# Performance work log

Hardware: AMD Instinct MI355X
Metric: run time of the kernel (lower is better)

## Reference

```python
import jax, jax.numpy as jnp
import numpy as np
from jax import lax

DN = ('NCHW', 'OIHW', 'NCHW')

def _hard_sigmoid(x):
    return jnp.clip(0.2 * x + 0.5, 0.0, 1.0)

def _conv(x, k, pad):
    return lax.conv_general_dilated(x, k, (1, 1), pad, dimension_numbers=DN)

def setup_inputs() -> dict:
    key = jax.random.key(0)
    k1, k2, k3 = jax.random.split(key, 3)
    B, T, C, H, W = 8, 16, 8, 128, 128
    F = 32
    x = jax.random.normal(k1, (B, T, C, H, W), dtype=jnp.float32)
    Wk = jax.random.normal(k2, (4 * F, C, 3, 3), dtype=jnp.float32) * 0.05
    Uk = jax.random.normal(k3, (4 * F, F, 3, 3), dtype=jnp.float32) * 0.05
    b = jnp.zeros((4 * F,), dtype=jnp.float32)
    return {"x": x, "Wk": Wk, "Uk": Uk, "b": b}

def reference(x, Wk, Uk, b):
    # ConvLSTM2D, channels_first, valid padding on input conv, same on recurrent conv,
    # gate order i,f,c,o; activation=tanh, recurrent_activation=hard_sigmoid.
    B, T, C, H, W = x.shape
    F = Uk.shape[1]
    kh, kw = Wk.shape[2], Wk.shape[3]
    Ho, Wo = H - kh + 1, W - kw + 1  # valid padding output spatial size
    bias = b[None, :, None, None]

    def step(carry, xt):
        h, c = carry
        z = _conv(xt, Wk, 'VALID') + _conv(h, Uk, 'SAME') + bias  # [B,4F,Ho,Wo]
        i, f, g, o = jnp.split(z, 4, axis=1)
        i = _hard_sigmoid(i)
        f = _hard_sigmoid(f)
        o = _hard_sigmoid(o)
        c_new = f * c + i * jnp.tanh(g)
        h_new = o * jnp.tanh(c_new)
        return (h_new, c_new), None

    h0 = jnp.zeros((B, F, Ho, Wo), dtype=x.dtype)
    c0 = jnp.zeros((B, F, Ho, Wo), dtype=x.dtype)
    xs = jnp.transpose(x, (1, 0, 2, 3, 4))  # [T,B,C,H,W]
    (hT, cT), _ = lax.scan(step, (h0, c0), xs)
    return hT  # return_sequences=False -> final hidden state [B,F,Ho,Wo]
```

## Files before the change

### kernel.cpp

```cpp
#include <hip/hip_runtime.h>
#include <hip/hip_bf16.h>

typedef __bf16 bf16_t;
typedef __attribute__((ext_vector_type(8))) __bf16 bf16x8;
typedef __attribute__((ext_vector_type(16))) float f32x16;
typedef unsigned int u32;

#define B_ 8
#define T_ 16
#define C_ 8
#define F_ 32
#define H_ 128
#define W_ 128
#define HO 126
#define WO 126
#define NKK 23
#define NBLK 256

#define BQ (NKK * 4096)
#define XS_OFF BQ
#define HS_OFF (BQ + 9792)
#define LDS_BYTES (BQ + 9792 + 39168)

__global__ __launch_bounds__(256) void prep_B(const float* __restrict__ Wk,
                                              const float* __restrict__ Uk,
                                              bf16_t* __restrict__ Bp) {
    int e = blockIdx.x * 256 + threadIdx.x;
    int j = e & 7, lane = (e >> 3) & 63, nt = (e >> 9) & 3, kk = e >> 11;
    int n = nt * 32 + (lane & 31), half = lane >> 5;
    float v = 0.f;
    if (kk < 5) {
        int p = 2 * kk + half, c = j;
        if (p <= 8) v = Wk[((n * C_ + c) * 3 + p / 3) * 3 + (p % 3)];
    } else {
        int kk2 = kk - 5, q = kk2 >> 1;
        int f = ((kk2 & 1) << 4) + (half << 3) + j;
        v = Uk[((n * F_ + f) * 3 + q / 3) * 3 + (q % 3)];
    }
    Bp[e] = (bf16_t)v;
}

__global__ __launch_bounds__(128) void conv_x(const float* __restrict__ x,
                                              bf16_t* __restrict__ xb) {
    const int tx = threadIdx.x;
    const int y = blockIdx.x, tb = blockIdx.y, bb = blockIdx.z;
    const float* xp = x + ((size_t)(bb * T_ + tb) * C_) * (H_ * W_) + y * W_ + tx;
    bf16x8 v;
    #pragma unroll
    for (int c = 0; c < 8; ++c) v[c] = (bf16_t)xp[(size_t)c * (H_ * W_)];
    *(bf16x8*)(xb + (((size_t)(bb * T_ + tb) * H_ + y) * W_ + tx) * 8) = v;
}

__global__ __launch_bounds__(512, 2) void lstm_persist(
    const bf16_t* __restrict__ xb,
    const bf16_t* __restrict__ Bp,
    const float* __restrict__ bias,
    bf16_t* __restrict__ g0,
    bf16_t* __restrict__ g1,
    float* __restrict__ cbuf,
    int* __restrict__ flags,
    int t0, int nsteps)
{
    __shared__ __align__(16) unsigned char smem[LDS_BYTES];
    const bool persist = (nsteps > 1);
    const int tid = threadIdx.x;
    const int w = tid >> 6, l = tid & 63;
    const int half = l >> 5;
    const int bid = blockIdx.x;
    const int bx = bid & 7, by = (bid >> 3) & 3, bb = bid >> 5;
    const int r0 = by * 32, c0 = bx * 16;

    for (int i = tid; i < BQ / 16; i += 512)
        *(bf16x8*)(smem + i * 16) = *(const bf16x8*)(Bp + i * 8);

    if (persist)
        for (int i = tid; i < 39168 / 4; i += 512)
            *(u32*)(smem + HS_OFF + i * 4) = 0u;

    const int fch = l & 31;
    float bv[4];
    #pragma unroll
    for (int n = 0; n < 4; ++n) bv[n] = bias[n * 32 + fch];

    const int trA = w * 4 + ((l & 31) >> 4);
    const int tcA = l & 15;
    const int baseX0 = XS_OFF + trA * 288 + tcA * 16;
    const int baseH0 = HS_OFF + half * 9792 + trA * 288 + tcA * 16;

    float* cbp = cbuf + (size_t)bb * (HO * WO * F_);
    float cre[2][16];
    #pragma unroll
    for (int m = 0; m < 2; ++m)
        #pragma unroll
        for (int r = 0; r < 16; ++r) {
            const int crow = (r & 3) + ((r >> 2) << 3) + (half << 2);
            const int px = w * 64 + m * 32 + crow;
            const int gy = r0 + (px >> 4), gx = c0 + (px & 15);
            cre[m][r] = (gy < HO && gx < WO) ? cbp[((size_t)gy * WO + gx) * F_ + fch] : 0.f;
        }

    constexpr int OFFT[10] = {0, 16, 32, 288, 304, 320, 576, 592, 608, 864};

    #pragma unroll 1
    for (int ts = 0; ts < nsteps; ++ts) {
        const int t = t0 + ts;
        bf16_t* Gcur = (t & 1) ? g1 : g0;
        const bf16_t* Gprev = (t & 1) ? g0 : g1;
        bf16_t* GcurB = Gcur + (size_t)bb * (HO * WO * F_);
        const u32* GprevW = (const u32*)(Gprev + (size_t)bb * (HO * WO * F_));

        const bf16_t* xt = xb + (size_t)(bb * T_ + t) * (H_ * W_ * 8);
        for (int i = tid; i < 612; i += 512) {
            int row = i / 18, col = i % 18;
            int gy = r0 + row, gx = c0 + col;
            bf16x8 v = {};
            if (gy < H_ && gx < W_) v = *(const bf16x8*)(xt + ((size_t)gy * W_ + gx) * 8);
            *(bf16x8*)(smem + XS_OFF + row * 288 + col * 16) = v;
        }

        if (!persist) {
            const bf16_t* hbR = Gprev + (size_t)bb * (HO * WO * F_);
            for (int i = tid; i < 2448; i += 512) {
                int pix = i >> 2, fg = i & 3;
                int row = pix / 18, col = pix % 18;
                int gy = r0 - 1 + row, gx = c0 - 1 + col;
                bf16x8 v = {};
                if (gy >= 0 && gy < HO && gx >= 0 && gx < WO)
                    v = *(const bf16x8*)(hbR + ((size_t)gy * WO + gx) * F_ + fg * 8);
                *(bf16x8*)(smem + HS_OFF + fg * 9792 + row * 288 + col * 16) = v;
            }
        }

        if (persist && ts > 0 && tid == 0) {
            #pragma unroll
            for (int dy = -1; dy <= 1; ++dy)
                #pragma unroll
                for (int dx = -1; dx <= 1; ++dx) {
                    if (dx == 0 && dy == 0) continue;
                    const int nx = bx + dx, ny = by + dy;
                    if (nx < 0 || nx > 7 || ny < 0 || ny > 3) continue;
                    const int nbid = (bb << 5) | (ny << 3) | nx;
                    int it = 0;
                    while (__hip_atomic_load(&flags[nbid * 32], __ATOMIC_RELAXED,
                                             __HIP_MEMORY_SCOPE_AGENT) < t &&
                           it < (1 << 15)) {
                        __builtin_amdgcn_s_sleep(2);
                        ++it;
                    }
                }
        }
        __syncthreads();

        if (persist && ts > 0) {
            for (int i = tid; i < 1600; i += 512) {
                int pid = i >> 4, ch2 = i & 15;
                int prow, pcol;
                if (pid < 18)      { prow = -1;        pcol = pid - 1; }
                else if (pid < 36) { prow = 32;        pcol = pid - 19; }
                else if (pid < 68) { prow = pid - 36;  pcol = -1; }
                else               { prow = pid - 68;  pcol = 16; }
                int gy = r0 + prow, gx = c0 + pcol;
                if (gy >= 0 && gy < HO && gx >= 0 && gx < WO) {
                    u32 v = __hip_atomic_load(&GprevW[(size_t)(gy * WO + gx) * 16 + ch2],
                                              __ATOMIC_RELAXED, __HIP_MEMORY_SCOPE_AGENT);
                    *(u32*)(smem + HS_OFF + (ch2 >> 2) * 9792 + (prow + 1) * 288 +
                            (pcol + 1) * 16 + (ch2 & 3) * 4) = v;
                }
            }
            __syncthreads();
        }

        f32x16 acc[2][4];
        #pragma unroll
        for (int m = 0; m < 2; ++m)
            #pragma unroll
            for (int n = 0; n < 4; ++n)
                #pragma unroll
                for (int j = 0; j < 16; ++j) acc[m][n][j] = bv[n];

        #pragma unroll
        for (int kk = 0; kk < NKK; ++kk) {
            int base0;
            if (kk < 5) {
                base0 = baseX0 + (half ? OFFT[2 * kk + 1] : OFFT[2 * kk]);
            } else {
                const int kk2 = kk - 5, q = kk2 >> 1, fgrp = kk2 & 1;
                base0 = baseH0 + fgrp * 19584 + (q / 3) * 288 + (q % 3) * 16;
            }
            bf16x8 a0 = *(const bf16x8*)(smem + base0);
            bf16x8 a1 = *(const bf16x8*)(smem + base0 + 576);
            const int bbo = kk * 4096 + l * 16;
            bf16x8 b0 = *(const bf16x8*)(smem + bbo);
            bf16x8 b1 = *(const bf16x8*)(smem + bbo + 1024);
            bf16x8 b2 = *(const bf16x8*)(smem + bbo + 2048);
            bf16x8 b3 = *(const bf16x8*)(smem + bbo + 3072);
            acc[0][0] = __builtin_amdgcn_mfma_f32_32x32x16_bf16(a0, b0, acc[0][0], 0, 0, 0);
            acc[0][1] = __builtin_amdgcn_mfma_f32_32x32x16_bf16(a0, b1, acc[0][1], 0, 0, 0);
            acc[0][2] = __builtin_amdgcn_mfma_f32_32x32x16_bf16(a0, b2, acc[0][2], 0, 0, 0);
            acc[0][3] = __builtin_amdgcn_mfma_f32_32x32x16_bf16(a0, b3, acc[0][3], 0, 0, 0);
            acc[1][0] = __builtin_amdgcn_mfma_f32_32x32x16_bf16(a1, b0, acc[1][0], 0, 0, 0);
            acc[1][1] = __builtin_amdgcn_mfma_f32_32x32x16_bf16(a1, b1, acc[1][1], 0, 0, 0);
            acc[1][2] = __builtin_amdgcn_mfma_f32_32x32x16_bf16(a1, b2, acc[1][2], 0, 0, 0);
            acc[1][3] = __builtin_amdgcn_mfma_f32_32x32x16_bf16(a1, b3, acc[1][3], 0, 0, 0);
        }
        __syncthreads();

        const bool last = (ts == nsteps - 1);
        #pragma unroll
        for (int m = 0; m < 2; ++m)
            #pragma unroll
            for (int r = 0; r < 16; ++r) {
                const int crow = (r & 3) + ((r >> 2) << 3) + (half << 2);
                const int px = w * 64 + m * 32 + crow;
                const int prow = px >> 4, pcol = px & 15;
                const int gy = r0 + prow, gx = c0 + pcol;
                const bool valid = (gy < HO && gx < WO);
                float zi = acc[m][0][r], zf = acc[m][1][r], zg = acc[m][2][r], zo = acc[m][3][r];
                float ig = fminf(fmaxf(0.2f * zi + 0.5f, 0.f), 1.f);
                float fg = fminf(fmaxf(0.2f * zf + 0.5f, 0.f), 1.f);
                float og = fminf(fmaxf(0.2f * zo + 0.5f, 0.f), 1.f);
                float eg = __expf(2.f * zg);
                float tg = 1.f - 2.f / (eg + 1.f);
                float cn = fg * cre[m][r] + ig * tg;
                cre[m][r] = cn;
                float ec = __expf(2.f * cn);
                float hn = og * (1.f - 2.f / (ec + 1.f));
                if (persist && !last) {
                    *(bf16_t*)(smem + HS_OFF + (fch >> 3) * 9792 + (prow + 1) * 288 +
                               (pcol + 1) * 16 + (fch & 7) * 2) = (bf16_t)(valid ? hn : 0.f);
                }
                if ((!persist || last) && valid)
                    GcurB[((size_t)gy * WO + gx) * F_ + fch] = (bf16_t)hn;
            }

        if (persist && !last) {
            __syncthreads();
            u32* GcurW = (u32*)GcurB;
            for (int i = tid; i < 1472; i += 512) {
                int pid = i >> 4, ch2 = i & 15;
                int prow, pcol;
                if (pid < 16)      { prow = 0;              pcol = pid; }
                else if (pid < 32) { prow = 31;             pcol = pid - 16; }
                else if (pid < 62) { prow = 1 + (pid - 32); pcol = 0; }
                else               { prow = 1 + (pid - 62); pcol = 15; }
                int gy = r0 + prow, gx = c0 + pcol;
                if (gy < HO && gx < WO) {
                    u32 v = *(u32*)(smem + HS_OFF + (ch2 >> 2) * 9792 + (prow + 1) * 288 +
                                    (pcol + 1) * 16 + (ch2 & 3) * 4);
                    __hip_atomic_store(&GcurW[(size_t)(gy * WO + gx) * 16 + ch2], v,
                                       __ATOMIC_RELAXED, __HIP_MEMORY_SCOPE_AGENT);
                }
            }
            __syncthreads();
            if (tid == 0)
                __hip_atomic_store(&flags[bid * 32], t + 1, __ATOMIC_RELAXED,
                                   __HIP_MEMORY_SCOPE_AGENT);
        }
    }

    #pragma unroll
    for (int m = 0; m < 2; ++m)
        #pragma unroll
        for (int r = 0; r < 16; ++r) {
            const int crow = (r & 3) + ((r >> 2) << 3) + (half << 2);
            const int px = w * 64 + m * 32 + crow;
            const int gy = r0 + (px >> 4), gx = c0 + (px & 15);
            if (gy < HO && gx < WO)
                cbp[((size_t)gy * WO + gx) * F_ + fch] = cre[m][r];
        }
}

__global__ __launch_bounds__(256) void out_transpose(const bf16_t* __restrict__ h,
                                                     float* __restrict__ out) {
    __shared__ float tile[WO * 33];
    const int gy = blockIdx.x, bb = blockIdx.y;
    const bf16_t* hp = h + ((size_t)bb * HO + gy) * (WO * F_);
    for (int i = threadIdx.x; i < WO * F_; i += 256) {
        int gx = i >> 5, f = i & 31;
        tile[gx * 33 + f] = (float)hp[i];
    }
    __syncthreads();
    float* op = out + (size_t)bb * (F_ * HO * WO) + (size_t)gy * WO;
    for (int i = threadIdx.x; i < WO * F_; i += 256) {
        int f = i / WO, gx = i % WO;
        op[(size_t)f * (HO * WO) + gx] = tile[gx * 33 + f];
    }
}

extern "C" void kernel_launch(void* const* d_in, const int* in_sizes, int n_in,
                              void* d_out, int out_size, void* d_ws, size_t ws_size,
                              hipStream_t stream) {
    const float* x    = (const float*)d_in[0];
    const float* Wk   = (const float*)d_in[1];
    const float* Uk   = (const float*)d_in[2];
    const float* bias = (const float*)d_in[3];
    float* out = (float*)d_out;

    const size_t N = (size_t)B_ * HO * WO * F_;
    bf16_t* g0p  = (bf16_t*)d_ws;
    bf16_t* g1p  = g0p + N;
    bf16_t* Bp   = g1p + N;
    bf16_t* xbuf = Bp + 47104;
    float*  cbuf = (float*)(xbuf + (size_t)16777216);
    int*    flg  = (int*)(cbuf + N);

    conv_x<<<dim3(H_, T_, B_), 128, 0, stream>>>(x, xbuf);
    prep_B<<<184, 256, 0, stream>>>(Wk, Uk, Bp);
    hipMemsetAsync(g1p, 0, N * sizeof(bf16_t), stream);
    hipMemsetAsync(cbuf, 0, N * sizeof(float), stream);
    hipMemsetAsync(flg, 0, NBLK * 32 * sizeof(int), stream);

    int t0 = 0, ns = T_;
    const bf16_t* xbc = xbuf;
    const bf16_t* Bpc = Bp;
    void* args[] = {(void*)&xbc, (void*)&Bpc, (void*)&bias, (void*)&g0p,
                    (void*)&g1p, (void*)&cbuf, (void*)&flg, (void*)&t0, (void*)&ns};
    hipError_t ce = hipLaunchCooperativeKernel((const void*)lstm_persist,
                                               dim3(NBLK), dim3(512), args, 0, stream);
    if (ce != hipSuccess) {
        for (int t = 0; t < T_; ++t) {
            int one = 1;
            lstm_persist<<<NBLK, 512, 0, stream>>>(xbuf, Bp, bias, g0p, g1p,
                                                   cbuf, flg, t, one);
        }
    }

    out_transpose<<<dim3(HO, B_), 256, 0, stream>>>(g1p, out);
}
```

Before: 581.0 us.

## Exchange tile halos through compact border buffer with 16-byte coherent loads

Instead of scattering per-dword relaxed atomic stores of border pixels into the full strided hidden-state array and gathering them back with atomic loads, each block now writes its 92 border pixels to a packed, double-buffered per-block border buffer using 16-byte stores with sc0 sc1 cache bits. Neighbours read their halo from that buffer with 16-byte coherent loads. The goal is fewer, wider, contiguous global transactions on the inter-block critical path of each timestep. In exchange it adds inline assembly, where each load waits on vmcnt(0) and so serialises, plus extra workspace indexing logic.

```diff
diff --git a/kernel.cpp b/kernel.cpp
--- a/kernel.cpp
+++ b/kernel.cpp
@@ -5,6 +5,7 @@
 typedef __attribute__((ext_vector_type(8))) __bf16 bf16x8;
 typedef __attribute__((ext_vector_type(16))) float f32x16;
 typedef unsigned int u32;
+typedef __attribute__((ext_vector_type(4))) u32 u32x4;
 
 #define B_ 8
 #define T_ 16
@@ -21,6 +22,16 @@
 #define XS_OFF BQ
 #define HS_OFF (BQ + 9792)
 #define LDS_BYTES (BQ + 9792 + 39168)
+
+__device__ __forceinline__ u32x4 load16_coherent(const void* p) {
+    u32x4 v;
+    asm volatile("global_load_dwordx4 %0, %1, off sc0 sc1\n\ts_waitcnt vmcnt(0)"
+                 : "=v"(v) : "v"(p) : "memory");
+    return v;
+}
+__device__ __forceinline__ void store16_coherent(void* p, u32x4 v) {
+    asm volatile("global_store_dwordx4 %0, %1, off sc0 sc1" :: "v"(p), "v"(v) : "memory");
+}
 
 __global__ __launch_bounds__(256) void prep_B(const float* __restrict__ Wk,
                                               const float* __restrict__ Uk,
@@ -57,6 +68,7 @@
     const float* __restrict__ bias,
     bf16_t* __restrict__ g0,
     bf16_t* __restrict__ g1,
+    bf16_t* __restrict__ bord,
     float* __restrict__ cbuf,
     int* __restrict__ flags,
     int t0, int nsteps)
@@ -107,7 +119,6 @@
         bf16_t* Gcur = (t & 1) ? g1 : g0;
         const bf16_t* Gprev = (t & 1) ? g0 : g1;
         bf16_t* GcurB = Gcur + (size_t)bb * (HO * WO * F_);
-        const u32* GprevW = (const u32*)(Gprev + (size_t)bb * (HO * WO * F_));
 
         const bf16_t* xt = xb + (size_t)(bb * T_ + t) * (H_ * W_ * 8);
         for (int i = tid; i < 612; i += 512) {
@@ -152,19 +163,28 @@
         __syncthreads();
 
         if (persist && ts > 0) {
-            for (int i = tid; i < 1600; i += 512) {
-                int pid = i >> 4, ch2 = i & 15;
+            if (tid < 400) {
+                const int pid = tid >> 2, quad = tid & 3;
                 int prow, pcol;
                 if (pid < 18)      { prow = -1;        pcol = pid - 1; }
                 else if (pid < 36) { prow = 32;        pcol = pid - 19; }
                 else if (pid < 68) { prow = pid - 36;  pcol = -1; }
                 else               { prow = pid - 68;  pcol = 16; }
-                int gy = r0 + prow, gx = c0 + pcol;
+                const int gy = r0 + prow, gx = c0 + pcol;
                 if (gy >= 0 && gy < HO && gx >= 0 && gx < WO) {
-                    u32 v = __hip_atomic_load(&GprevW[(size_t)(gy * WO + gx) * 16 + ch2],
-                                              __ATOMIC_RELAXED, __HIP_MEMORY_SCOPE_AGENT);
-                    *(u32*)(smem + HS_OFF + (ch2 >> 2) * 9792 + (prow + 1) * 288 +
-                            (pcol + 1) * 16 + (ch2 & 3) * 4) = v;
+                    const int oby = gy >> 5, obx = gx >> 4;
+                    const int opr = gy & 31, opc = gx & 15;
+                    int opid;
+                    if (opr == 0)       opid = opc;
+                    else if (opr == 31) opid = 16 + opc;
+                    else if (opc == 0)  opid = 32 + (opr - 1);
+                    else                opid = 62 + (opr - 1);
+                    const int nbid = (bb << 5) | (oby << 3) | obx;
+                    const bf16_t* src = bord +
+                        ((((size_t)((t + 1) & 1) * NBLK + nbid) * 92 + opid) * 4 + quad) * 8;
+                    u32x4 v = load16_coherent(src);
+                    *(u32x4*)(smem + HS_OFF + quad * 9792 + (prow + 1) * 288 +
+                              (pcol + 1) * 16) = v;
                 }
             }
             __syncthreads();
@@ -235,21 +255,18 @@
 
         if (persist && !last) {
             __syncthreads();
-            u32* GcurW = (u32*)GcurB;
-            for (int i = tid; i < 1472; i += 512) {
-                int pid = i >> 4, ch2 = i & 15;
+            if (tid < 368) {
+                const int pid = tid >> 2, quad = tid & 3;
                 int prow, pcol;
                 if (pid < 16)      { prow = 0;              pcol = pid; }
                 else if (pid < 32) { prow = 31;             pcol = pid - 16; }
                 else if (pid < 62) { prow = 1 + (pid - 32); pcol = 0; }
                 else               { prow = 1 + (pid - 62); pcol = 15; }
-                int gy = r0 + prow, gx = c0 + pcol;
-                if (gy < HO && gx < WO) {
-                    u32 v = *(u32*)(smem + HS_OFF + (ch2 >> 2) * 9792 + (prow + 1) * 288 +
-                                    (pcol + 1) * 16 + (ch2 & 3) * 4);
-                    __hip_atomic_store(&GcurW[(size_t)(gy * WO + gx) * 16 + ch2], v,
-                                       __ATOMIC_RELAXED, __HIP_MEMORY_SCOPE_AGENT);
-                }
+                u32x4 v = *(const u32x4*)(smem + HS_OFF + quad * 9792 +
+                                          (prow + 1) * 288 + (pcol + 1) * 16);
+                bf16_t* dst = bord +
+                    ((((size_t)(t & 1) * NBLK + bid) * 92 + pid) * 4 + quad) * 8;
+                store16_coherent(dst, v);
             }
             __syncthreads();
             if (tid == 0)
@@ -303,6 +320,7 @@
     bf16_t* xbuf = Bp + 47104;
     float*  cbuf = (float*)(xbuf + (size_t)16777216);
     int*    flg  = (int*)(cbuf + N);
+    bf16_t* bord = (bf16_t*)(flg + NBLK * 32);
 
     conv_x<<<dim3(H_, T_, B_), 128, 0, stream>>>(x, xbuf);
     prep_B<<<184, 256, 0, stream>>>(Wk, Uk, Bp);
@@ -314,14 +332,15 @@
     const bf16_t* xbc = xbuf;
     const bf16_t* Bpc = Bp;
     void* args[] = {(void*)&xbc, (void*)&Bpc, (void*)&bias, (void*)&g0p,
-                    (void*)&g1p, (void*)&cbuf, (void*)&flg, (void*)&t0, (void*)&ns};
+                    (void*)&g1p, (void*)&bord, (void*)&cbuf, (void*)&flg,
+                    (void*)&t0, (void*)&ns};
     hipError_t ce = hipLaunchCooperativeKernel((const void*)lstm_persist,
                                                dim3(NBLK), dim3(512), args, 0, stream);
     if (ce != hipSuccess) {
         for (int t = 0; t < T_; ++t) {
             int one = 1;
             lstm_persist<<<NBLK, 512, 0, stream>>>(xbuf, Bp, bias, g0p, g1p,
-                                                   cbuf, flg, t, one);
+                                                   bord, cbuf, flg, t, one);
         }
     }
 
```

New measurement: 606.8 us. 1.04x slower.
